# Kernel tuning notes

Measured on AMD Instinct MI355X. Metric: run time of the kernel, lower is better.

Reference implementation:

```python
import jax, jax.numpy as jnp
import numpy as np

B, NR_BOX, D = 512, 18, 2048
NR_OBJ = NR_BOX - 2
K = 3
NUM_CLASSES = 174
NUM_CAT = 321


def setup_inputs() -> dict:
    key = jax.random.key(0)
    k1, k2, k3, k4, k5, k6 = jax.random.split(key, 6)
    obj_fea = jax.random.normal(k1, (B, NR_BOX, D), dtype=jnp.float32)
    # cooccurrence: nonnegative, sparse-ish, first (pad) column zero as in the torch code
    cooc = jax.random.uniform(k2, (NUM_CLASSES, NUM_CAT), dtype=jnp.float32)
    mask = jax.random.uniform(k3, (NUM_CLASSES, NUM_CAT)) < 0.5
    cooc = jnp.where(mask, cooc, 0.0).at[:, 0].set(0.0)
    obj_indicator = jax.random.randint(k4, (B, NR_BOX), 0, 2).astype(jnp.int32)
    obj_category = jax.random.randint(k5, (B, NR_BOX), 0, NUM_CAT).astype(jnp.int32)
    labels = jax.random.randint(k6, (B,), 0, NUM_CLASSES).astype(jnp.int32)
    return {
        'obj_fea': obj_fea,
        'cooccurrence': cooc,
        'obj_indicator': obj_indicator,
        'obj_category': obj_category,
        'labels': labels,
    }


def reference(obj_fea, cooccurrence, obj_indicator, obj_category, labels):
    Bn, nr_box, d = obj_fea.shape
    nr_obj = nr_box - 2
    ind = obj_indicator[:, 2:]          # (B, nr_obj)
    cats = obj_category[:, 2:]          # (B, nr_obj)
    ori_comp = obj_fea.mean(axis=1)     # (B, d)
    objs = obj_fea[:, 2:]               # (B, nr_obj, d), hands dropped
    label_onehot = jax.nn.one_hot(labels, NUM_CLASSES, dtype=obj_fea.dtype)  # (B, C)

    # W[i, b, j] = cooccurrence[labels[i], cats[b, j]]  (candidate weights per sample i)
    cooc_lab = cooccurrence[labels]                 # (B, NUM_CAT)
    W = cooc_lab[:, cats]                           # (B, B, nr_obj)
    eye = jnp.eye(Bn, dtype=bool)
    W = jnp.where(eye[:, :, None], 0.0, W)          # exclude own video (cand_obj[i] = 0)
    Wf = W.reshape(Bn, Bn * nr_obj)

    # softmax(log w) over nonzero support == w / sum(w); sample via categorical on log-weights
    logits = jnp.where(Wf > 0, jnp.log(jnp.where(Wf > 0, Wf, 1.0)), -jnp.inf)
    has_cand = (Wf > 0).any(axis=1) & (ind != 0).any(axis=1)  # (B,)

    rng = jax.random.key(42)
    r1, r2, r3 = jax.random.split(rng, 3)
    sel = jax.random.categorical(r1, logits, shape=(K, Bn)).T   # (B, K) flat candidate ids
    batch_idx = sel // nr_obj
    box_idx = sel % nr_obj
    sel_fea = objs[batch_idx, box_idx]              # (B, K, d)
    sel_label = label_onehot[batch_idx]             # (B, K, C)

    lam = jax.random.uniform(r2, (Bn, 1, 1), dtype=obj_fea.dtype)  # Beta(1,1)==U(0,1), one per sample
    slots = jax.random.randint(r3, (Bn, K), 0, nr_obj)
    own_fea = jnp.take_along_axis(objs, slots[:, :, None], axis=1)  # (B, K, d)

    mixed_fea = own_fea * lam + sel_fea * (1.0 - lam)
    mixed_label = label_onehot[:, None, :] * lam + sel_label * (1.0 - lam)

    # fallback path: mean of own objects + own one-hot label, repeated K times
    fb_fea = jnp.broadcast_to(objs.mean(axis=1)[:, None, :], mixed_fea.shape)
    fb_label = jnp.broadcast_to(label_onehot[:, None, :], mixed_label.shape)
    m = has_cand[:, None, None]
    mix_fea = jnp.where(m, mixed_fea, fb_fea)
    mix_label = jnp.where(m, mixed_label, fb_label)
    return ori_comp, mix_fea, mix_label
```

## Files before the change

kernel.cpp:

```cpp
#include <hip/hip_runtime.h>
#include <stdint.h>
#include <math.h>

#define NBOX 18
#define BB 512
#define DD 2048
#define NOBJ 16
#define KK 3
#define NCLS 174
#define NCAT 321
#define NQ 4
#define QCAND 2048
#define TINYF 1.1754943508222875e-38f

__host__ __device__ __forceinline__ uint32_t rotl32(uint32_t x, int d) {
  return (x << d) | (x >> (32 - d));
}

__host__ __device__ __forceinline__ void threefry2x32(uint32_t k0, uint32_t k1,
                                                      uint32_t x0, uint32_t x1,
                                                      uint32_t& o0, uint32_t& o1) {
  uint32_t ks2 = k0 ^ k1 ^ 0x1BD11BDAu;
  x0 += k0; x1 += k1;
#define TFR(r) x0 += x1; x1 = rotl32(x1, r); x1 ^= x0;
#define R4A TFR(13) TFR(15) TFR(26) TFR(6)
#define R4B TFR(17) TFR(29) TFR(16) TFR(24)
  R4A x0 += k1;  x1 += ks2 + 1u;
  R4B x0 += ks2; x1 += k0 + 2u;
  R4A x0 += k0;  x1 += k1 + 3u;
  R4B x0 += k1;  x1 += ks2 + 4u;
  R4A x0 += ks2; x1 += k0 + 5u;
#undef R4A
#undef R4B
#undef TFR
  o0 = x0; o1 = x1;
}

__device__ __forceinline__ float bits_to_unit(uint32_t bits) {
  float f = __uint_as_float((bits >> 9) | 0x3f800000u);
  return f - 1.0f;
}

__global__ __launch_bounds__(256) void fused_sample_ori(
    const float* __restrict__ obj_fea, const float* __restrict__ cooc,
    const int* __restrict__ obj_cat, const int* __restrict__ labels,
    uint32_t r1h, uint32_t r1l,
    unsigned long long* __restrict__ part, int* __restrict__ cnts,
    float* __restrict__ ori, float4* __restrict__ s16ws) {
  const int gb = blockIdx.x;
  const int b = gb >> 2;
  const int q = gb & 3;
  const int tid = threadIdx.x;
  const int lane = tid & 63;
  const int wid = tid >> 6;

  __shared__ unsigned short jl[QCAND];
  __shared__ float wl[QCAND];
  __shared__ float pv[KK * 4];
  __shared__ int pj[KK * 4];
  __shared__ int wc[4];
  __shared__ float4 xch[128];

  const int lab = labels[b];
  const float* crow = cooc + (size_t)lab * NCAT;
  const int seg = wid << 9;
  const int jbase = (q << 11) + seg;
  int cnt = 0;
#pragma unroll 1
  for (int c = 0; c < 8; ++c) {
    int j = jbase + (c << 6) + lane;
    int jb = j >> 4;
    float w = 0.0f;
    if (jb != b) w = crow[obj_cat[jb * NBOX + 2 + (j & 15)]];
    unsigned long long m = __ballot(w > 0.0f);
    if (w > 0.0f) {
      int rank = __popcll(m & ((1ull << lane) - 1ull));
      jl[seg + cnt + rank] = (unsigned short)j;
      wl[seg + cnt + rank] = w;
    }
    cnt += __popcll(m);
  }
  if (lane == 0) wc[wid] = cnt;

  const int col = tid & 127;
  const int half = tid >> 7;
  const float4* fea4 = (const float4*)obj_fea;
  const size_t lbase = ((size_t)b * NBOX + half * 9) * 512 + (q << 7) + col;
  float4 a0 = fea4[lbase];
  float4 a1 = fea4[lbase + 512];
  float4 a2 = fea4[lbase + 2 * 512];
  float4 a3 = fea4[lbase + 3 * 512];
  float4 a4 = fea4[lbase + 4 * 512];
  float4 a5 = fea4[lbase + 5 * 512];
  float4 a6 = fea4[lbase + 6 * 512];
  float4 a7 = fea4[lbase + 7 * 512];
  float4 a8 = fea4[lbase + 8 * 512];
  __builtin_amdgcn_sched_barrier(0);

#pragma unroll 1
  for (int k = 0; k < KK; ++k) {
    uint32_t cbase = ((uint32_t)(k * BB + b)) << 13;
    float br = 0.0f;
    int bj = 0;
    for (int p = lane; p < cnt; p += 64) {
      uint32_t j = jl[seg + p];
      float w = wl[seg + p];
      uint32_t t0, t1;
      threefry2x32(r1h, r1l, 0u, cbase + j, t0, t1);
      float u = bits_to_unit(t0 ^ t1);
      if (u == 0.0f) u = TINYF;
      float t = -logf(u);
      if (w > br * t) { br = w / t; bj = (int)j; }
    }
#pragma unroll
    for (int mm = 1; mm < 64; mm <<= 1) {
      float ov = __shfl_xor(br, mm, 64);
      int oj = __shfl_xor(bj, mm, 64);
      if (ov > br || (ov == br && oj < bj)) { br = ov; bj = oj; }
    }
    if (lane == 0) { pv[k * 4 + wid] = br; pj[k * 4 + wid] = bj; }
  }
  __syncthreads();

  if (tid == 0) {
    cnts[gb] = wc[0] + wc[1] + wc[2] + wc[3];
#pragma unroll
    for (int k = 0; k < KK; ++k) {
      float bv = pv[k * 4]; int bj = pj[k * 4];
      for (int w4 = 1; w4 < 4; ++w4) {
        float vv = pv[k * 4 + w4]; int jj = pj[k * 4 + w4];
        if (vv > bv || (vv == bv && jj < bj)) { bv = vv; bj = jj; }
      }
      part[((size_t)b * KK + k) * NQ + q] =
          ((unsigned long long)__float_as_uint(bv) << 32) | (uint32_t)(8192 - bj);
    }
  }

  float4 A;
  A.x = a0.x + a1.x + a2.x + a3.x + a4.x + a5.x + a6.x + a7.x + a8.x;
  A.y = a0.y + a1.y + a2.y + a3.y + a4.y + a5.y + a6.y + a7.y + a8.y;
  A.z = a0.z + a1.z + a2.z + a3.z + a4.z + a5.z + a6.z + a7.z + a8.z;
  A.w = a0.w + a1.w + a2.w + a3.w + a4.w + a5.w + a6.w + a7.w + a8.w;
  if (half) xch[col] = A;
  __syncthreads();
  if (!half) {
    float4 Bv = xch[col];
    float4 S = make_float4(A.x + Bv.x, A.y + Bv.y, A.z + Bv.z, A.w + Bv.w);
    const float is = 1.0f / 18.0f;
    const size_t oidx = (size_t)b * 512 + (q << 7) + col;
    ((float4*)ori)[oidx] = make_float4(S.x * is, S.y * is, S.z * is, S.w * is);
    s16ws[oidx] = make_float4(S.x - a0.x - a1.x, S.y - a0.y - a1.y,
                              S.z - a0.z - a1.z, S.w - a0.w - a1.w);
  }
}

__global__ __launch_bounds__(256) void mix_kernel(
    const float* __restrict__ obj_fea, const int* __restrict__ obj_ind,
    const int* __restrict__ labels,
    const unsigned long long* __restrict__ part, const int* __restrict__ cnts,
    const float4* __restrict__ s16ws,
    uint32_t r2h, uint32_t r2l, uint32_t r3bh, uint32_t r3bl,
    float* __restrict__ mixf, float* __restrict__ mixl) {
  const int bx = blockIdx.x;
  const int b = bx >> 1;
  const int h = bx & 1;
  const int tid = threadIdx.x;
  const int off = (h << 8) + tid;

  __shared__ int s_sel[KK];
  __shared__ int s_slots[KK];
  __shared__ float s_lam;
  __shared__ int s_hc;
  if (tid < KK) {
    const int k = tid;
    unsigned long long best = part[((size_t)b * KK + k) * NQ];
#pragma unroll
    for (int qq = 1; qq < NQ; ++qq) {
      unsigned long long p = part[((size_t)b * KK + k) * NQ + qq];
      if (p > best) best = p;
    }
    s_sel[k] = 8192 - (int)(best & 0xFFFFFFFFull);
    uint32_t s0, s1;
    threefry2x32(r3bh, r3bl, 0u, (uint32_t)(b * KK + k), s0, s1);
    s_slots[k] = (int)((s0 ^ s1) & 15u);
  } else if (tid == 3) {
    int tot = cnts[b * NQ] + cnts[b * NQ + 1] + cnts[b * NQ + 2] + cnts[b * NQ + 3];
    int any = 0;
#pragma unroll
    for (int o = 0; o < NOBJ; ++o) any |= (obj_ind[b * NBOX + 2 + o] != 0);
    s_hc = (tot > 0) && any;
  } else if (tid == 4) {
    uint32_t c0, c1;
    threefry2x32(r2h, r2l, 0u, (uint32_t)b, c0, c1);
    s_lam = bits_to_unit(c0 ^ c1);
  }
  __syncthreads();

  const int hc = s_hc;
  const float l = s_lam, l1 = 1.0f - l;
  const float4* fea4 = (const float4*)obj_fea;
  float4* mixf4 = (float4*)mixf;
  if (hc) {
#pragma unroll 1
    for (int k = 0; k < KK; ++k) {
      int s = s_sel[k];
      int bi = s >> 4, bo = s & 15, sl = s_slots[k];
      float4 a = fea4[((size_t)b * NBOX + 2 + sl) * 512 + off];
      float4 e = fea4[((size_t)bi * NBOX + 2 + bo) * 512 + off];
      float4 o;
      o.x = a.x * l + e.x * l1; o.y = a.y * l + e.y * l1;
      o.z = a.z * l + e.z * l1; o.w = a.w * l + e.w * l1;
      mixf4[((size_t)b * KK + k) * 512 + off] = o;
    }
  } else {
    float4 s16 = s16ws[(size_t)b * 512 + off];
    const float is = 1.0f / 16.0f;
    float4 o = make_float4(s16.x * is, s16.y * is, s16.z * is, s16.w * is);
#pragma unroll
    for (int k = 0; k < KK; ++k) mixf4[((size_t)b * KK + k) * 512 + off] = o;
  }

  if (h == 0 && tid < NCLS) {
    int lb = labels[b];
#pragma unroll 1
    for (int k = 0; k < KK; ++k) {
      float val;
      if (hc) {
        int ls = labels[s_sel[k] >> 4];
        val = (tid == lb ? l : 0.0f) + (tid == ls ? l1 : 0.0f);
      } else {
        val = (tid == lb) ? 1.0f : 0.0f;
      }
      mixl[(size_t)(b * KK + k) * NCLS + tid] = val;
    }
  }
}

extern "C" void kernel_launch(void* const* d_in, const int* in_sizes, int n_in,
                              void* d_out, int out_size, void* d_ws, size_t ws_size,
                              hipStream_t stream) {
  (void)in_sizes; (void)n_in; (void)out_size; (void)ws_size;
  const float* obj_fea = (const float*)d_in[0];
  const float* cooc    = (const float*)d_in[1];
  const int* obj_ind   = (const int*)d_in[2];
  const int* obj_cat   = (const int*)d_in[3];
  const int* labels    = (const int*)d_in[4];

  float* out  = (float*)d_out;
  float* ori  = out;
  float* mixf = out + (size_t)BB * DD;
  float* mixl = mixf + (size_t)BB * KK * DD;

  char* ws = (char*)d_ws;
  unsigned long long* part = (unsigned long long*)ws;
  int* cnts = (int*)(ws + (size_t)BB * KK * NQ * 8);
  float4* s16ws = (float4*)(ws + 64 * 1024);

  uint32_t r1h, r1l, r2h, r2l, r3h, r3l;
  threefry2x32(0u, 42u, 0u, 0u, r1h, r1l);
  threefry2x32(0u, 42u, 0u, 1u, r2h, r2l);
  threefry2x32(0u, 42u, 0u, 2u, r3h, r3l);
  uint32_t r3bh, r3bl;
  threefry2x32(r3h, r3l, 0u, 1u, r3bh, r3bl);

  hipLaunchKernelGGL(fused_sample_ori, dim3(BB * NQ), dim3(256), 0, stream,
                     obj_fea, cooc, obj_cat, labels, r1h, r1l,
                     part, cnts, ori, s16ws);
  hipLaunchKernelGGL(mix_kernel, dim3(BB * 2), dim3(256), 0, stream,
                     obj_fea, obj_ind, labels, part, cnts, s16ws,
                     r2h, r2l, r3bh, r3bl, mixf, mixl);
}
```

Before: 43.03 us.

## Fuse K sampling loops, stage cooccurrence row in LDS, drop block-level partial reduction

The three categorical draws are now computed in a single pass over the compacted candidate list, so jl/wl are read once and three independent threefry chains can be interleaved for ILP. The cooccurrence row is copied into per-wave LDS before the candidate gather, replacing scattered global reads. Per-wave partial maxima and counts go straight to global memory (16 partials per sample), which removes a __syncthreads and the single-thread reduction but makes the mix kernel reduce more partials. The workspace offsets are enlarged to fit the larger partial arrays.

```diff
diff --git a/kernel.cpp b/kernel.cpp
--- a/kernel.cpp
+++ b/kernel.cpp
@@ -11,6 +11,7 @@
 #define NCAT 321
 #define NQ 4
 #define QCAND 2048
+#define NPART 16
 #define TINYF 1.1754943508222875e-38f
 
 __host__ __device__ __forceinline__ uint32_t rotl32(uint32_t x, int d) {
@@ -56,31 +57,8 @@
 
   __shared__ unsigned short jl[QCAND];
   __shared__ float wl[QCAND];
-  __shared__ float pv[KK * 4];
-  __shared__ int pj[KK * 4];
-  __shared__ int wc[4];
+  __shared__ float scrow[4 * 336];
   __shared__ float4 xch[128];
-
-  const int lab = labels[b];
-  const float* crow = cooc + (size_t)lab * NCAT;
-  const int seg = wid << 9;
-  const int jbase = (q << 11) + seg;
-  int cnt = 0;
-#pragma unroll 1
-  for (int c = 0; c < 8; ++c) {
-    int j = jbase + (c << 6) + lane;
-    int jb = j >> 4;
-    float w = 0.0f;
-    if (jb != b) w = crow[obj_cat[jb * NBOX + 2 + (j & 15)]];
-    unsigned long long m = __ballot(w > 0.0f);
-    if (w > 0.0f) {
-      int rank = __popcll(m & ((1ull << lane) - 1ull));
-      jl[seg + cnt + rank] = (unsigned short)j;
-      wl[seg + cnt + rank] = w;
-    }
-    cnt += __popcll(m);
-  }
-  if (lane == 0) wc[wid] = cnt;
 
   const int col = tid & 127;
   const int half = tid >> 7;
@@ -97,43 +75,69 @@
   float4 a8 = fea4[lbase + 8 * 512];
   __builtin_amdgcn_sched_barrier(0);
 
-#pragma unroll 1
-  for (int k = 0; k < KK; ++k) {
-    uint32_t cbase = ((uint32_t)(k * BB + b)) << 13;
-    float br = 0.0f;
-    int bj = 0;
-    for (int p = lane; p < cnt; p += 64) {
-      uint32_t j = jl[seg + p];
-      float w = wl[seg + p];
-      uint32_t t0, t1;
-      threefry2x32(r1h, r1l, 0u, cbase + j, t0, t1);
-      float u = bits_to_unit(t0 ^ t1);
-      if (u == 0.0f) u = TINYF;
-      float t = -logf(u);
-      if (w > br * t) { br = w / t; bj = (int)j; }
-    }
-#pragma unroll
-    for (int mm = 1; mm < 64; mm <<= 1) {
-      float ov = __shfl_xor(br, mm, 64);
-      int oj = __shfl_xor(bj, mm, 64);
-      if (ov > br || (ov == br && oj < bj)) { br = ov; bj = oj; }
-    }
-    if (lane == 0) { pv[k * 4 + wid] = br; pj[k * 4 + wid] = bj; }
-  }
-  __syncthreads();
-
-  if (tid == 0) {
-    cnts[gb] = wc[0] + wc[1] + wc[2] + wc[3];
-#pragma unroll
-    for (int k = 0; k < KK; ++k) {
-      float bv = pv[k * 4]; int bj = pj[k * 4];
-      for (int w4 = 1; w4 < 4; ++w4) {
-        float vv = pv[k * 4 + w4]; int jj = pj[k * 4 + w4];
-        if (vv > bv || (vv == bv && jj < bj)) { bv = vv; bj = jj; }
-      }
-      part[((size_t)b * KK + k) * NQ + q] =
-          ((unsigned long long)__float_as_uint(bv) << 32) | (uint32_t)(8192 - bj);
-    }
+  const int lab = labels[b];
+  const float* crow = cooc + (size_t)lab * NCAT;
+  const int cbase_lds = wid * 336;
+  for (int i = lane; i < NCAT; i += 64) scrow[cbase_lds + i] = crow[i];
+
+  const int seg = wid << 9;
+  const int jbase = (q << 11) + seg;
+  int cnt = 0;
+#pragma unroll 1
+  for (int c = 0; c < 8; ++c) {
+    int j = jbase + (c << 6) + lane;
+    int jb = j >> 4;
+    float w = 0.0f;
+    if (jb != b) w = scrow[cbase_lds + obj_cat[jb * NBOX + 2 + (j & 15)]];
+    unsigned long long m = __ballot(w > 0.0f);
+    if (w > 0.0f) {
+      int rank = __popcll(m & ((1ull << lane) - 1ull));
+      jl[seg + cnt + rank] = (unsigned short)j;
+      wl[seg + cnt + rank] = w;
+    }
+    cnt += __popcll(m);
+  }
+
+  const uint32_t cbase0 = ((uint32_t)b) << 13;
+  const uint32_t kstep = 1u << 22;
+  float br0 = 0.f, br1 = 0.f, br2 = 0.f;
+  int bj0 = 0, bj1 = 0, bj2 = 0;
+#pragma unroll 1
+  for (int p = lane; p < cnt; p += 64) {
+    uint32_t j = jl[seg + p];
+    float w = wl[seg + p];
+    uint32_t cc = cbase0 + j;
+    uint32_t x0, x1, y0, y1, z0, z1;
+    threefry2x32(r1h, r1l, 0u, cc, x0, x1);
+    threefry2x32(r1h, r1l, 0u, cc + kstep, y0, y1);
+    threefry2x32(r1h, r1l, 0u, cc + 2u * kstep, z0, z1);
+    float t0 = -logf(fmaxf(bits_to_unit(x0 ^ x1), TINYF));
+    float t1 = -logf(fmaxf(bits_to_unit(y0 ^ y1), TINYF));
+    float t2 = -logf(fmaxf(bits_to_unit(z0 ^ z1), TINYF));
+    if (w > br0 * t0) { br0 = w / t0; bj0 = (int)j; }
+    if (w > br1 * t1) { br1 = w / t1; bj1 = (int)j; }
+    if (w > br2 * t2) { br2 = w / t2; bj2 = (int)j; }
+  }
+#pragma unroll
+  for (int mm = 1; mm < 64; mm <<= 1) {
+    float ov; int oj;
+    ov = __shfl_xor(br0, mm, 64); oj = __shfl_xor(bj0, mm, 64);
+    if (ov > br0 || (ov == br0 && oj < bj0)) { br0 = ov; bj0 = oj; }
+    ov = __shfl_xor(br1, mm, 64); oj = __shfl_xor(bj1, mm, 64);
+    if (ov > br1 || (ov == br1 && oj < bj1)) { br1 = ov; bj1 = oj; }
+    ov = __shfl_xor(br2, mm, 64); oj = __shfl_xor(bj2, mm, 64);
+    if (ov > br2 || (ov == br2 && oj < bj2)) { br2 = ov; bj2 = oj; }
+  }
+  if (lane == 0) {
+    const int pw = q * 4 + wid;
+    const size_t pb = (size_t)b * KK * NPART;
+    part[pb + 0 * NPART + pw] =
+        ((unsigned long long)__float_as_uint(br0) << 32) | (uint32_t)(8192 - bj0);
+    part[pb + 1 * NPART + pw] =
+        ((unsigned long long)__float_as_uint(br1) << 32) | (uint32_t)(8192 - bj1);
+    part[pb + 2 * NPART + pw] =
+        ((unsigned long long)__float_as_uint(br2) << 32) | (uint32_t)(8192 - bj2);
+    cnts[b * NPART + pw] = cnt;
   }
 
   float4 A;
@@ -173,18 +177,21 @@
   __shared__ int s_hc;
   if (tid < KK) {
     const int k = tid;
-    unsigned long long best = part[((size_t)b * KK + k) * NQ];
-#pragma unroll
-    for (int qq = 1; qq < NQ; ++qq) {
-      unsigned long long p = part[((size_t)b * KK + k) * NQ + qq];
-      if (p > best) best = p;
+    const unsigned long long* pp = part + ((size_t)b * KK + k) * NPART;
+    unsigned long long best = pp[0];
+#pragma unroll
+    for (int p = 1; p < NPART; ++p) {
+      unsigned long long v = pp[p];
+      if (v > best) best = v;
     }
     s_sel[k] = 8192 - (int)(best & 0xFFFFFFFFull);
     uint32_t s0, s1;
     threefry2x32(r3bh, r3bl, 0u, (uint32_t)(b * KK + k), s0, s1);
     s_slots[k] = (int)((s0 ^ s1) & 15u);
   } else if (tid == 3) {
-    int tot = cnts[b * NQ] + cnts[b * NQ + 1] + cnts[b * NQ + 2] + cnts[b * NQ + 3];
+    int tot = 0;
+#pragma unroll
+    for (int p = 0; p < NPART; ++p) tot += cnts[b * NPART + p];
     int any = 0;
 #pragma unroll
     for (int o = 0; o < NOBJ; ++o) any |= (obj_ind[b * NBOX + 2 + o] != 0);
@@ -253,8 +260,8 @@
 
   char* ws = (char*)d_ws;
   unsigned long long* part = (unsigned long long*)ws;
-  int* cnts = (int*)(ws + (size_t)BB * KK * NQ * 8);
-  float4* s16ws = (float4*)(ws + 64 * 1024);
+  int* cnts = (int*)(ws + (size_t)BB * KK * NPART * 8);
+  float4* s16ws = (float4*)(ws + 256 * 1024);
 
   uint32_t r1h, r1l, r2h, r2l, r3h, r3l;
   threefry2x32(0u, 42u, 0u, 0u, r1h, r1l);
```

Measured after the change: 48.47 us. 12.6% more time.
